# Optimization experiments

Measured on AMD Instinct MI355X. Metric: run time of the kernel, lower is better.

Reference implementation:

```python
import jax, jax.numpy as jnp
import numpy as np

NEG = 1e12  # matches the torch '-inf' surrogate value


def _sinusoidal_pos(seq_len, dim):
    # bert4keras-style: pe[..., 0::2] = sin, pe[..., 1::2] = cos
    pos = jnp.arange(seq_len, dtype=jnp.float32)
    i = jnp.arange(dim // 2, dtype=jnp.float32)
    freq = jnp.power(10000.0, -2.0 * i / dim)
    ang = pos[:, None] * freq[None, :]                      # [S, dim/2]
    pe = jnp.stack([jnp.sin(ang), jnp.cos(ang)], axis=-1)   # [S, dim/2, 2]
    return pe.reshape(seq_len, dim)                          # [S, dim]


def _rope(e, cos_pos, sin_pos):
    # additional_part = stack([-e[...,1::2], e[...,::2]], -1).reshape(e.shape)
    rot = jnp.stack([-e[..., 1::2], e[..., 0::2]], axis=-1).reshape(e.shape)
    return e * cos_pos + rot * sin_pos


def setup_inputs() -> dict:
    key = jax.random.key(0)
    k = jax.random.split(key, 5)
    B, S, H, inner, L = 8, 512, 768, 64, 16
    x = jax.random.normal(k[0], (B, S, H), dtype=jnp.float32)
    W1 = jax.random.normal(k[1], (H, 2 * inner), dtype=jnp.float32) * 0.02
    b1 = jnp.zeros((2 * inner,), dtype=jnp.float32)
    W2 = jax.random.normal(k[2], (H, 2 * L), dtype=jnp.float32) * 0.02
    b2 = jnp.zeros((2 * L,), dtype=jnp.float32)
    attention_mask = jnp.ones((B, S), dtype=jnp.int32)
    return {"x": x, "W1": W1, "b1": b1, "W2": W2, "b2": b2,
            "attention_mask": attention_mask}


def reference(x, W1, b1, W2, b2, attention_mask):
    B, S, H = x.shape
    inner = W1.shape[1] // 2

    t = x @ W1 + b1                                 # [B,S,2*inner]
    start_token = t[..., 0::2]                      # [B,S,inner]
    end_token = t[..., 1::2]                        # [B,S,inner]

    pe = _sinusoidal_pos(S, inner)[None]            # [1,S,inner]
    cos_pos = jnp.repeat(pe[..., 1::2], 2, axis=-1)
    sin_pos = jnp.repeat(pe[..., 0::2], 2, axis=-1)
    start_token = _rope(start_token, cos_pos, sin_pos)
    end_token = _rope(end_token, cos_pos, sin_pos)

    span_score = jnp.einsum('bmd,bnd->bmn', start_token, end_token) / (inner ** 0.5)

    typing = jnp.swapaxes(x @ W2 + b2, 1, 2) / 2.0  # [B,2L,S]

    # entity_score: [B, L, S(start), S(end)]
    entity_score = (span_score[:, None]
                    + typing[:, 0::2, None, :]
                    + typing[:, 1::2, :, None])

    m = attention_mask.astype(entity_score.dtype)
    m_row = m[:, None, :, None]                     # mask over start axis
    m_col = m[:, None, None, :]                     # mask over end axis
    entity_score = entity_score * m_row + (-NEG) * (1.0 - m_row)
    entity_score = entity_score * m_col + (-NEG) * (1.0 - m_col)

    tril = jnp.tril(jnp.ones((S, S), entity_score.dtype), k=-1)
    entity_score = entity_score - tril * NEG
    return entity_score
```

## Files before the change

### kernel.cpp

```cpp
#include <hip/hip_runtime.h>

#define NEGF 1.0e12f

constexpr int Hdim = 768;
constexpr int NC   = 160;
constexpr int ROWS = 4096;
constexpr int SEQ  = 512;
constexpr int KSPLIT = 4;

typedef __attribute__((ext_vector_type(8))) short  short8;
typedef __attribute__((ext_vector_type(4))) float  floatx4;

__device__ inline unsigned short f2bf(float f) {
    union { float f; unsigned u; } v; v.f = f;
    return (unsigned short)((v.u + 0x8000u) >> 16);
}

__global__ __launch_bounds__(256) void gemm_mfma_k(
    const float* __restrict__ x, const float* __restrict__ W1,
    const float* __restrict__ W2, float* __restrict__ partial)
{
    __shared__ __align__(16) unsigned short xs[64 * 40];
    __shared__ __align__(16) unsigned short ws[NC * 40];

    const int tid  = threadIdx.x;
    const int wave = tid >> 6;
    const int lane = tid & 63;
    const int quad = lane >> 4;
    const int nl   = lane & 15;
    const int r0   = blockIdx.x * 64;
    const int k0   = blockIdx.y * 192;

    floatx4 acc[10];
#pragma unroll
    for (int t = 0; t < 10; t++) acc[t] = (floatx4)(0.0f);

    for (int kt = 0; kt < 192; kt += 32) {
        const int kb = k0 + kt;
        {
            const int row = tid >> 2;
            const int kq  = (tid & 3) * 8;
            const float* xp = x + (size_t)(r0 + row) * Hdim + kb + kq;
            float4 v0 = *(const float4*)xp;
            float4 v1 = *(const float4*)(xp + 4);
            short8 sv;
            sv[0] = (short)f2bf(v0.x); sv[1] = (short)f2bf(v0.y);
            sv[2] = (short)f2bf(v0.z); sv[3] = (short)f2bf(v0.w);
            sv[4] = (short)f2bf(v1.x); sv[5] = (short)f2bf(v1.y);
            sv[6] = (short)f2bf(v1.z); sv[7] = (short)f2bf(v1.w);
            *(short8*)(xs + row * 40 + kq) = sv;
        }
#pragma unroll
        for (int g = 0; g < 3; g++) {
            const int c   = g * 64 + (tid & 63);
            const int kq2 = (tid >> 6) * 8;
            if (c < NC) {
                float f[8];
                if (c < 128) {
                    const float* wp = W1 + (size_t)(kb + kq2) * 128 + c;
#pragma unroll
                    for (int j = 0; j < 8; j++) f[j] = wp[j * 128];
                } else {
                    const float* wp = W2 + (size_t)(kb + kq2) * 32 + (c - 128);
#pragma unroll
                    for (int j = 0; j < 8; j++) f[j] = wp[j * 32];
                }
                short8 sv;
#pragma unroll
                for (int j = 0; j < 8; j++) sv[j] = (short)f2bf(f[j]);
                *(short8*)(ws + c * 40 + kq2) = sv;
            }
        }
        __syncthreads();

        short8 af = *(const short8*)(xs + (wave * 16 + nl) * 40 + quad * 8);
#pragma unroll
        for (int t = 0; t < 10; t++) {
            short8 bf = *(const short8*)(ws + (t * 16 + nl) * 40 + quad * 8);
            acc[t] = __builtin_amdgcn_mfma_f32_16x16x32_bf16(af, bf, acc[t], 0, 0, 0);
        }
        __syncthreads();
    }

    float* pout = partial + (size_t)blockIdx.y * ROWS * NC;
#pragma unroll
    for (int t = 0; t < 10; t++) {
#pragma unroll
        for (int r = 0; r < 4; r++) {
            pout[(size_t)(r0 + wave * 16 + quad * 4 + r) * NC + t * 16 + nl] = acc[t][r];
        }
    }
}

__global__ __launch_bounds__(256) void combine_rope_k(
    const float* __restrict__ partial, const float* __restrict__ b1,
    const float* __restrict__ b2, unsigned short* __restrict__ startbf,
    unsigned short* __restrict__ endbf, float* __restrict__ tyn,
    float* __restrict__ tym)
{
    const int tid = threadIdx.x;
    const int row = blockIdx.x * 4 + (tid >> 6);
    const int u   = tid & 63;
    const int b   = row >> 9;
    const int s   = row & 511;
    const float* p0 = partial + (size_t)row * NC;
    const size_t cstride = (size_t)ROWS * NC;

    if (u < 32) {
        const int i = u;
        float4 a0 = *(const float4*)(p0 + 4 * i);
        float4 a1 = *(const float4*)(p0 + cstride + 4 * i);
        float4 a2 = *(const float4*)(p0 + 2 * cstride + 4 * i);
        float4 a3 = *(const float4*)(p0 + 3 * cstride + 4 * i);
        float t0 = a0.x + a1.x + a2.x + a3.x + b1[4 * i + 0];
        float t1 = a0.y + a1.y + a2.y + a3.y + b1[4 * i + 1];
        float t2 = a0.z + a1.z + a2.z + a3.z + b1[4 * i + 2];
        float t3 = a0.w + a1.w + a2.w + a3.w + b1[4 * i + 3];
        float freq = __powf(10000.0f, -(float)i * (1.0f / 32.0f));
        float ang  = (float)s * freq;
        float sn, cs;
        __sincosf(ang, &sn, &cs);
        float so0 = (t0 * cs - t2 * sn) * 0.125f;
        float so1 = (t2 * cs + t0 * sn) * 0.125f;
        float eo0 = t1 * cs - t3 * sn;
        float eo1 = t3 * cs + t1 * sn;
        ushort2 sp; sp.x = f2bf(so0); sp.y = f2bf(so1);
        ushort2 ep; ep.x = f2bf(eo0); ep.y = f2bf(eo1);
        *(ushort2*)(startbf + (size_t)row * 64 + 2 * i) = sp;
        *(ushort2*)(endbf   + (size_t)row * 64 + 2 * i) = ep;
    } else {
        const int j = u - 32;
        float t = p0[128 + j] + p0[cstride + 128 + j] + p0[2 * cstride + 128 + j]
                + p0[3 * cstride + 128 + j] + b2[j];
        float v = t * 0.5f;
        const int l = j >> 1;
        if ((j & 1) == 0) tyn[((size_t)b * 16 + l) * SEQ + s] = v;
        else              tym[((size_t)b * 16 + l) * SEQ + s] = v;
    }
}

__global__ __launch_bounds__(256) void entity_k(
    const unsigned short* __restrict__ startbf, const unsigned short* __restrict__ endbf,
    const float* __restrict__ tyn, const float* __restrict__ tym,
    const int* __restrict__ amask, float* __restrict__ out)
{
    __shared__ __align__(16) unsigned short sA[64 * 72];
    __shared__ __align__(16) unsigned short sB[64 * 72];
    __shared__ float tyn_s[16 * 64];
    __shared__ float tym_s[16 * 64];
    __shared__ float mrow_s[64];
    __shared__ float mcol_s[64];

    const int tid = threadIdx.x;
    const int b   = blockIdx.z;
    const int m0  = blockIdx.y * 64;
    const int n0  = blockIdx.x * 64;

    for (int t = tid; t < 512; t += 256) {
        int row = t >> 3;
        int kq  = (t & 7) * 8;
        *(short8*)(sA + row * 72 + kq) =
            *(const short8*)(startbf + (size_t)(b * SEQ + m0 + row) * 64 + kq);
        *(short8*)(sB + row * 72 + kq) =
            *(const short8*)(endbf + (size_t)(b * SEQ + n0 + row) * 64 + kq);
    }
    for (int t = tid; t < 16 * 64; t += 256) {
        int l = t >> 6, i = t & 63;
        tym_s[t] = tym[((size_t)b * 16 + l) * SEQ + m0 + i];
        tyn_s[t] = tyn[((size_t)b * 16 + l) * SEQ + n0 + i];
    }
    if (tid < 64)       mrow_s[tid] = (float)amask[b * SEQ + m0 + tid];
    else if (tid < 128) mcol_s[tid - 64] = (float)amask[b * SEQ + n0 + (tid - 64)];
    __syncthreads();

    const int wave = tid >> 6;
    const int lane = tid & 63;
    const int quad = lane >> 4;
    const int nl   = lane & 15;

    short8 a0 = *(const short8*)(sA + (wave * 16 + nl) * 72 + quad * 8);
    short8 a1 = *(const short8*)(sA + (wave * 16 + nl) * 72 + 32 + quad * 8);

    floatx4 acc[4];
#pragma unroll
    for (int t = 0; t < 4; t++) acc[t] = (floatx4)(0.0f);
#pragma unroll
    for (int t = 0; t < 4; t++) {
        short8 bf0 = *(const short8*)(sB + (t * 16 + nl) * 72 + quad * 8);
        short8 bf1 = *(const short8*)(sB + (t * 16 + nl) * 72 + 32 + quad * 8);
        acc[t] = __builtin_amdgcn_mfma_f32_16x16x32_bf16(a0, bf0, acc[t], 0, 0, 0);
        acc[t] = __builtin_amdgcn_mfma_f32_16x16x32_bf16(a1, bf1, acc[t], 0, 0, 0);
    }

    float mr[4], radd[4];
#pragma unroll
    for (int r = 0; r < 4; r++) {
        mr[r]   = mrow_s[wave * 16 + quad * 4 + r];
        radd[r] = -NEGF * (1.0f - mr[r]);
    }
    float mc[4], cadd[4];
#pragma unroll
    for (int t = 0; t < 4; t++) {
        mc[t]   = mcol_s[t * 16 + nl];
        cadd[t] = -NEGF * (1.0f - mc[t]);
    }
    const bool lower = (m0 > n0);
    const bool diag  = (m0 == n0);
    const int  lm    = wave * 16 + quad * 4;

    for (int l = 0; l < 16; l++) {
        float tmv[4];
#pragma unroll
        for (int r = 0; r < 4; r++) tmv[r] = tym_s[l * 64 + lm + r];
        float* ob = out + ((size_t)(b * 16 + l) * SEQ + m0 + lm) * SEQ + n0;
#pragma unroll
        for (int t = 0; t < 4; t++) {
            float tnv = tyn_s[l * 64 + t * 16 + nl];
#pragma unroll
            for (int r = 0; r < 4; r++) {
                float v = acc[t][r] + tnv + tmv[r];
                v = v * mr[r] + radd[r];
                v = v * mc[t] + cadd[t];
                if (lower) v -= NEGF;
                else if (diag && (lm + r > t * 16 + nl)) v -= NEGF;
                ob[(size_t)r * SEQ + t * 16 + nl] = v;
            }
        }
    }
}

extern "C" void kernel_launch(void* const* d_in, const int* in_sizes, int n_in,
                              void* d_out, int out_size, void* d_ws, size_t ws_size,
                              hipStream_t stream) {
    const float* x     = (const float*)d_in[0];
    const float* W1    = (const float*)d_in[1];
    const float* b1    = (const float*)d_in[2];
    const float* W2    = (const float*)d_in[3];
    const float* b2    = (const float*)d_in[4];
    const int*   amask = (const int*)d_in[5];
    float* out = (float*)d_out;

    char* base = (char*)d_ws;
    float*          partial = (float*)base;
    unsigned short* startbf = (unsigned short*)(base + 10485760);
    unsigned short* endbf   = (unsigned short*)(base + 10485760 + 524288);
    float*          tyn     = (float*)(base + 10485760 + 2 * 524288);
    float*          tym     = (float*)(base + 10485760 + 2 * 524288 + 262144);

    hipLaunchKernelGGL(gemm_mfma_k, dim3(64, KSPLIT), dim3(256), 0, stream,
                       x, W1, W2, partial);
    hipLaunchKernelGGL(combine_rope_k, dim3(ROWS / 4), dim3(256), 0, stream,
                       partial, b1, b2, startbf, endbf, tyn, tym);
    hipLaunchKernelGGL(entity_k, dim3(8, 8, 8), dim3(256), 0, stream,
                       startbf, endbf, tyn, tym, amask, out);
}
```

Baseline: 169.7 us.

## Restructure entity kernel to full-row tiles with vectorized stores and causal MFMA skip

```diff
diff --git a/kernel.cpp b/kernel.cpp
--- a/kernel.cpp
+++ b/kernel.cpp
@@ -139,92 +139,95 @@
     }
 }
 
-__global__ __launch_bounds__(256) void entity_k(
+__global__ __launch_bounds__(256) void entity_fused_k(
     const unsigned short* __restrict__ startbf, const unsigned short* __restrict__ endbf,
     const float* __restrict__ tyn, const float* __restrict__ tym,
     const int* __restrict__ amask, float* __restrict__ out)
 {
-    __shared__ __align__(16) unsigned short sA[64 * 72];
-    __shared__ __align__(16) unsigned short sB[64 * 72];
-    __shared__ float tyn_s[16 * 64];
-    __shared__ float tym_s[16 * 64];
-    __shared__ float mrow_s[64];
-    __shared__ float mcol_s[64];
-
-    const int tid = threadIdx.x;
-    const int b   = blockIdx.z;
-    const int m0  = blockIdx.y * 64;
-    const int n0  = blockIdx.x * 64;
-
-    for (int t = tid; t < 512; t += 256) {
-        int row = t >> 3;
-        int kq  = (t & 7) * 8;
-        *(short8*)(sA + row * 72 + kq) =
-            *(const short8*)(startbf + (size_t)(b * SEQ + m0 + row) * 64 + kq);
-        *(short8*)(sB + row * 72 + kq) =
-            *(const short8*)(endbf + (size_t)(b * SEQ + n0 + row) * 64 + kq);
-    }
-    for (int t = tid; t < 16 * 64; t += 256) {
-        int l = t >> 6, i = t & 63;
-        tym_s[t] = tym[((size_t)b * 16 + l) * SEQ + m0 + i];
-        tyn_s[t] = tyn[((size_t)b * 16 + l) * SEQ + n0 + i];
-    }
-    if (tid < 64)       mrow_s[tid] = (float)amask[b * SEQ + m0 + tid];
-    else if (tid < 128) mcol_s[tid - 64] = (float)amask[b * SEQ + n0 + (tid - 64)];
-    __syncthreads();
-
+    __shared__ __align__(16) float span_s[16 * 516];
+    __shared__ __align__(16) float tyn_s[8 * SEQ];
+    __shared__ float tym_s[8 * 16];
+
+    const int tid  = threadIdx.x;
+    const int m0   = blockIdx.x * 16;
+    const int lh   = blockIdx.y;
+    const int b    = blockIdx.z;
     const int wave = tid >> 6;
     const int lane = tid & 63;
     const int quad = lane >> 4;
     const int nl   = lane & 15;
 
-    short8 a0 = *(const short8*)(sA + (wave * 16 + nl) * 72 + quad * 8);
-    short8 a1 = *(const short8*)(sA + (wave * 16 + nl) * 72 + 32 + quad * 8);
-
-    floatx4 acc[4];
-#pragma unroll
-    for (int t = 0; t < 4; t++) acc[t] = (floatx4)(0.0f);
-#pragma unroll
-    for (int t = 0; t < 4; t++) {
-        short8 bf0 = *(const short8*)(sB + (t * 16 + nl) * 72 + quad * 8);
-        short8 bf1 = *(const short8*)(sB + (t * 16 + nl) * 72 + 32 + quad * 8);
-        acc[t] = __builtin_amdgcn_mfma_f32_16x16x32_bf16(a0, bf0, acc[t], 0, 0, 0);
-        acc[t] = __builtin_amdgcn_mfma_f32_16x16x32_bf16(a1, bf1, acc[t], 0, 0, 0);
-    }
-
-    float mr[4], radd[4];
-#pragma unroll
-    for (int r = 0; r < 4; r++) {
-        mr[r]   = mrow_s[wave * 16 + quad * 4 + r];
-        radd[r] = -NEGF * (1.0f - mr[r]);
-    }
-    float mc[4], cadd[4];
-#pragma unroll
-    for (int t = 0; t < 4; t++) {
-        mc[t]   = mcol_s[t * 16 + nl];
-        cadd[t] = -NEGF * (1.0f - mc[t]);
-    }
-    const bool lower = (m0 > n0);
-    const bool diag  = (m0 == n0);
-    const int  lm    = wave * 16 + quad * 4;
-
-    for (int l = 0; l < 16; l++) {
-        float tmv[4];
-#pragma unroll
-        for (int r = 0; r < 4; r++) tmv[r] = tym_s[l * 64 + lm + r];
-        float* ob = out + ((size_t)(b * 16 + l) * SEQ + m0 + lm) * SEQ + n0;
-#pragma unroll
-        for (int t = 0; t < 4; t++) {
-            float tnv = tyn_s[l * 64 + t * 16 + nl];
-#pragma unroll
-            for (int r = 0; r < 4; r++) {
-                float v = acc[t][r] + tnv + tmv[r];
-                v = v * mr[r] + radd[r];
-                v = v * mc[t] + cadd[t];
-                if (lower) v -= NEGF;
-                else if (diag && (lm + r > t * 16 + nl)) v -= NEGF;
-                ob[(size_t)r * SEQ + t * 16 + nl] = v;
+    const unsigned short* ap = startbf + ((size_t)(b * SEQ + m0 + nl)) * 64 + quad * 8;
+    short8 a0 = *(const short8*)ap;
+    short8 a1 = *(const short8*)(ap + 32);
+
+    floatx4 acc[8];
+#pragma unroll
+    for (int t = 0; t < 8; t++) acc[t] = (floatx4)(0.0f);
+#pragma unroll
+    for (int t = 0; t < 8; t++) {
+        if (wave * 128 + t * 16 + 15 >= m0) {
+            const unsigned short* ep =
+                endbf + ((size_t)(b * SEQ + wave * 128 + t * 16 + nl)) * 64 + quad * 8;
+            short8 bf0 = *(const short8*)ep;
+            short8 bf1 = *(const short8*)(ep + 32);
+            acc[t] = __builtin_amdgcn_mfma_f32_16x16x32_bf16(a0, bf0, acc[t], 0, 0, 0);
+            acc[t] = __builtin_amdgcn_mfma_f32_16x16x32_bf16(a1, bf1, acc[t], 0, 0, 0);
+        }
+    }
+
+    {
+        const floatx4* src = (const floatx4*)(tyn + ((size_t)b * 16 + lh * 8) * SEQ);
+        for (int t = tid; t < 8 * SEQ / 4; t += 256) ((floatx4*)tyn_s)[t] = src[t];
+        if (tid < 128) {
+            const int l = tid >> 4, r = tid & 15;
+            tym_s[tid] = tym[((size_t)b * 16 + lh * 8 + l) * SEQ + m0 + r];
+        }
+    }
+#pragma unroll
+    for (int t = 0; t < 8; t++)
+#pragma unroll
+        for (int r = 0; r < 4; r++)
+            span_s[(quad * 4 + r) * 516 + wave * 128 + t * 16 + nl] = acc[t][r];
+    __syncthreads();
+
+    const int row = tid >> 4;
+    const int uu  = tid & 15;
+    const int m   = m0 + row;
+    const float mr   = (float)amask[b * SEQ + m];
+    const float radd = -NEGF * (1.0f - mr);
+
+    floatx4 spanz[8], mcv[8], caddv[8];
+#pragma unroll
+    for (int q = 0; q < 8; q++) {
+        spanz[q] = *(const floatx4*)(span_s + row * 516 + uu * 4 + q * 64);
+        const int4 mk = *(const int4*)(amask + b * SEQ + uu * 4 + q * 64);
+        const int mki[4] = {mk.x, mk.y, mk.z, mk.w};
+#pragma unroll
+        for (int e = 0; e < 4; e++) {
+            const int n = uu * 4 + q * 64 + e;
+            float mc = (float)mki[e];
+            mcv[q][e] = mc;
+            float ca = -NEGF * (1.0f - mc);
+            caddv[q][e] = (n < m) ? (ca - NEGF) : ca;
+        }
+    }
+
+    for (int l = 0; l < 8; l++) {
+        const float tm = tym_s[l * 16 + row];
+        float* orow = out + (((size_t)(b * 16 + lh * 8 + l)) * SEQ + m) * SEQ;
+#pragma unroll
+        for (int q = 0; q < 8; q++) {
+            floatx4 t4 = *(const floatx4*)(tyn_s + l * SEQ + uu * 4 + q * 64);
+            floatx4 v;
+#pragma unroll
+            for (int e = 0; e < 4; e++) {
+                float xv = spanz[q][e] + t4[e] + tm;
+                xv = xv * mr + radd;
+                xv = xv * mcv[q][e] + caddv[q][e];
+                v[e] = xv;
             }
+            *(floatx4*)(orow + uu * 4 + q * 64) = v;
         }
     }
 }
@@ -251,6 +254,6 @@
                        x, W1, W2, partial);
     hipLaunchKernelGGL(combine_rope_k, dim3(ROWS / 4), dim3(256), 0, stream,
                        partial, b1, b2, startbf, endbf, tyn, tym);
-    hipLaunchKernelGGL(entity_k, dim3(8, 8, 8), dim3(256), 0, stream,
+    hipLaunchKernelGGL(entity_fused_k, dim3(32, 2, 8), dim3(256), 0, stream,
                        startbf, endbf, tyn, tym, amask, out);
 }
```

Result: no change. 170.7 us (+0.5%).
